# Performance work log

Hardware: AMD Instinct MI355X
Metric: run time of the kernel (lower is better)

The kernel has to match this reference:

```python
import jax, jax.numpy as jnp
import numpy as np

B = 8192
INPUT_DIM = 1024
HIDDEN = 4096
LATENT = 256
K = 16384  # codebook size
COMMIT = 0.25


def setup_inputs() -> dict:
    key = jax.random.key(0)
    ks = jax.random.split(key, 12)

    def lin(k, fan_in, fan_out):
        bound = 1.0 / np.sqrt(fan_in)
        kw, kb = jax.random.split(k)
        W = jax.random.uniform(kw, (fan_in, fan_out), jnp.float32, -bound, bound)
        b = jax.random.uniform(kb, (fan_out,), jnp.float32, -bound, bound)
        return W, b

    eW1, eb1 = lin(ks[0], INPUT_DIM, HIDDEN)
    eW2, eb2 = lin(ks[1], HIDDEN, HIDDEN)
    eW3, eb3 = lin(ks[2], HIDDEN, LATENT)
    dW1, db1 = lin(ks[3], LATENT, HIDDEN)
    dW2, db2 = lin(ks[4], HIDDEN, HIDDEN)
    dW3, db3 = lin(ks[5], HIDDEN, INPUT_DIM)
    codebook = jax.random.uniform(ks[6], (K, LATENT), jnp.float32, -1.0 / K, 1.0 / K)
    x = jax.random.normal(ks[7], (B, INPUT_DIM), jnp.float32)
    return {
        "x": x,
        "eW1": eW1, "eb1": eb1, "eW2": eW2, "eb2": eb2, "eW3": eW3, "eb3": eb3,
        "codebook": codebook,
        "dW1": dW1, "db1": db1, "dW2": dW2, "db2": db2, "dW3": dW3, "db3": db3,
    }


def _encoder(x, eW1, eb1, eW2, eb2, eW3, eb3):
    h = jax.nn.relu(x @ eW1 + eb1)          # dropout is identity in eval
    h = jax.nn.relu(h @ eW2 + eb2)
    return jnp.tanh(h @ eW3 + eb3)          # [B, LATENT]


def _decoder(z, dW1, db1, dW2, db2, dW3, db3):
    h = jax.nn.relu(z @ dW1 + db1)
    h = jax.nn.relu(h @ dW2 + db2)
    return h @ dW3 + db3                    # [B, INPUT_DIM]


def _vq(z, codebook):
    # pairwise squared distances: ||z||^2 + ||e||^2 - 2 z.e^T   -> [B, K]
    d = (jnp.sum(z * z, axis=1, keepdims=True)
         + jnp.sum(codebook * codebook, axis=1)
         - 2.0 * (z @ codebook.T))
    idx = jnp.argmin(d, axis=1)                              # [B]
    enc = jax.nn.one_hot(idx, K, dtype=jnp.float32)          # [B, K]
    q = enc @ codebook                                       # [B, LATENT]
    e_loss = jnp.mean((jax.lax.stop_gradient(q) - z) ** 2)
    q_loss = jnp.mean((q - jax.lax.stop_gradient(z)) ** 2)
    vq_loss = q_loss + COMMIT * e_loss
    q_st = z + jax.lax.stop_gradient(q - z)                  # straight-through
    avg_probs = jnp.mean(enc, axis=0)
    perplexity = jnp.exp(-jnp.sum(avg_probs * jnp.log(avg_probs + 1e-10)))
    return q_st, idx, vq_loss, perplexity


def reference(x, eW1, eb1, eW2, eb2, eW3, eb3, codebook,
              dW1, db1, dW2, db2, dW3, db3):
    z = _encoder(x, eW1, eb1, eW2, eb2, eW3, eb3)
    q, tokens, vq_loss, perplexity = _vq(z, codebook)
    recon = _decoder(q, dW1, db1, dW2, db2, dW3, db3)
    recon_loss = jnp.mean((recon - x) ** 2)
    total = vq_loss + recon_loss
    return recon, tokens, vq_loss, recon_loss, total, perplexity
```

## Files before the change

### kernel.cpp

```cpp
#include <hip/hip_runtime.h>
#include <stdint.h>

#define B_N 8192
#define D_IN 1024
#define D_HID 4096
#define D_LAT 256
#define K_CB 16384

typedef __attribute__((ext_vector_type(8))) short bf16x8;
typedef __attribute__((ext_vector_type(4))) float f32x4;

__device__ __forceinline__ unsigned short f2b(float v) {
  unsigned u = __float_as_uint(v);
  u += 0x7fffu + ((u >> 16) & 1u);
  return (unsigned short)(u >> 16);
}

__global__ __launch_bounds__(256, 2) void enc_big_k(
    const float* __restrict__ A, const float* __restrict__ Bm,
    const float* __restrict__ bias, float* __restrict__ C, int M, int N,
    int K) {
  __shared__ float As[16 * 260];
  __shared__ float Bs[16 * 128];
  const int tid = threadIdx.x;
  const int w = tid >> 6;
  const int tx = tid & 15, ty = tid >> 4;
  int bx = blockIdx.x, by = blockIdx.y;
  {
    const int gx = gridDim.x, n = gx * gridDim.y;
    const int wg = by * gx + bx;
    const int q = n >> 3;
    const int s = (wg & 7) * q + (wg >> 3);
    bx = s % gx;
    by = s / gx;
  }
  const int m0 = by << 8, n0 = bx << 7;

  float acc[16][8];
#pragma unroll
  for (int i = 0; i < 16; ++i)
#pragma unroll
    for (int j = 0; j < 8; ++j) acc[i][j] = 0.0f;

  for (int k0 = 0; k0 < K; k0 += 16) {
#pragma unroll
    for (int r = 0; r < 4; ++r) {
      const int f = tid + (r << 8);
      const int m = f >> 2, kq = (f & 3) << 2;
      const float4 v = *(const float4*)(A + (size_t)(m0 + m) * K + k0 + kq);
      As[(kq + 0) * 260 + m] = v.x;
      As[(kq + 1) * 260 + m] = v.y;
      As[(kq + 2) * 260 + m] = v.z;
      As[(kq + 3) * 260 + m] = v.w;
    }
#pragma unroll
    for (int r = 0; r < 2; ++r) {
      const int f = tid + (r << 8);
      const float* gp = Bm + (size_t)(k0 + (f >> 5)) * N + n0 + ((f & 31) << 2);
      __builtin_amdgcn_global_load_lds((const unsigned int*)gp,
                                       (unsigned int*)&Bs[(r << 10) + (w << 8)],
                                       16, 0, 0);
    }
    __syncthreads();
#pragma unroll
    for (int kk = 0; kk < 16; ++kk) {
      float a[16], b[8];
#pragma unroll
      for (int q = 0; q < 4; ++q)
        *(float4*)(a + (q << 2)) =
            *(const float4*)(&As[kk * 260 + (q << 6) + (ty << 2)]);
      *(float4*)(b) = *(const float4*)(&Bs[kk * 128 + (tx << 2)]);
      *(float4*)(b + 4) = *(const float4*)(&Bs[kk * 128 + 64 + (tx << 2)]);
#pragma unroll
      for (int i = 0; i < 16; ++i)
#pragma unroll
        for (int j = 0; j < 8; ++j) acc[i][j] = fmaf(a[i], b[j], acc[i][j]);
    }
    __syncthreads();
  }

  float bb[8];
  *(float4*)(bb) = *(const float4*)(bias + n0 + (tx << 2));
  *(float4*)(bb + 4) = *(const float4*)(bias + n0 + 64 + (tx << 2));
#pragma unroll
  for (int i = 0; i < 16; ++i) {
    const int row = m0 + ((i >> 2) << 6) + (ty << 2) + (i & 3);
    float vrow[8];
#pragma unroll
    for (int j = 0; j < 8; ++j) vrow[j] = fmaxf(acc[i][j] + bb[j], 0.0f);
    *(float4*)(C + (size_t)row * N + n0 + (tx << 2)) = *(float4*)(vrow);
    *(float4*)(C + (size_t)row * N + n0 + 64 + (tx << 2)) = *(float4*)(vrow + 4);
  }
}

__global__ __launch_bounds__(256, 2) void enc_small_k(
    const float* __restrict__ A, const float* __restrict__ Bm,
    const float* __restrict__ bias, float* __restrict__ C, int M, int N,
    int K) {
  __shared__ float As[16][128];
  __shared__ float Bs[16][128];
  const int tid = threadIdx.x;
  const int tx = tid & 15, ty = tid >> 4;
  const int m0 = blockIdx.y << 7, n0 = blockIdx.x << 7;
  float acc[8][8];
#pragma unroll
  for (int i = 0; i < 8; ++i)
#pragma unroll
    for (int j = 0; j < 8; ++j) acc[i][j] = 0.0f;
  for (int k0 = 0; k0 < K; k0 += 16) {
#pragma unroll
    for (int r = 0; r < 2; ++r) {
      const int f = tid + (r << 8);
      const int m = f >> 2, kq = (f & 3) << 2;
      const float4 v = *(const float4*)(A + (size_t)(m0 + m) * K + k0 + kq);
      As[kq + 0][m] = v.x; As[kq + 1][m] = v.y;
      As[kq + 2][m] = v.z; As[kq + 3][m] = v.w;
    }
#pragma unroll
    for (int r = 0; r < 2; ++r) {
      const int f = tid + (r << 8);
      const int k = f >> 5, nq = (f & 31) << 2;
      *(float4*)(&Bs[k][nq]) =
          *(const float4*)(Bm + (size_t)(k0 + k) * N + n0 + nq);
    }
    __syncthreads();
#pragma unroll
    for (int kk = 0; kk < 16; ++kk) {
      float a[8], b[8];
      *(float4*)(a) = *(const float4*)(&As[kk][ty << 2]);
      *(float4*)(a + 4) = *(const float4*)(&As[kk][64 + (ty << 2)]);
      *(float4*)(b) = *(const float4*)(&Bs[kk][tx << 2]);
      *(float4*)(b + 4) = *(const float4*)(&Bs[kk][64 + (tx << 2)]);
#pragma unroll
      for (int i = 0; i < 8; ++i)
#pragma unroll
        for (int j = 0; j < 8; ++j) acc[i][j] = fmaf(a[i], b[j], acc[i][j]);
    }
    __syncthreads();
  }
  float bb[8];
  *(float4*)(bb) = *(const float4*)(bias + n0 + (tx << 2));
  *(float4*)(bb + 4) = *(const float4*)(bias + n0 + 64 + (tx << 2));
#pragma unroll
  for (int i = 0; i < 8; ++i) {
    const int row = m0 + ((i < 4) ? (ty << 2) + i : 64 + (ty << 2) + i - 4);
    float vrow[8];
#pragma unroll
    for (int j = 0; j < 8; ++j) vrow[j] = fmaxf(acc[i][j] + bb[j], 0.0f);
    *(float4*)(C + (size_t)row * N + n0 + (tx << 2)) = *(float4*)(vrow);
    *(float4*)(C + (size_t)row * N + n0 + 64 + (tx << 2)) = *(float4*)(vrow + 4);
  }
}

__global__ __launch_bounds__(256, 2) void enc3_part_k(
    const float* __restrict__ A, const float* __restrict__ B,
    float* __restrict__ P, int M, int K) {
  __shared__ float As[16][128];
  __shared__ float Bs[16][128];
  const int tid = threadIdx.x;
  const int tx = tid & 15, ty = tid >> 4;
  const int m0 = blockIdx.y << 7, n0 = blockIdx.x << 7;
  const int s = blockIdx.z;
  const int kbeg = s * (K >> 2), kend = kbeg + (K >> 2);
  float acc[8][8];
#pragma unroll
  for (int i = 0; i < 8; ++i)
#pragma unroll
    for (int j = 0; j < 8; ++j) acc[i][j] = 0.0f;
  for (int k0 = kbeg; k0 < kend; k0 += 16) {
#pragma unroll
    for (int r = 0; r < 2; ++r) {
      const int f = tid + (r << 8);
      const int m = f >> 2, kq = (f & 3) << 2;
      const float4 v = *(const float4*)(A + (size_t)(m0 + m) * K + k0 + kq);
      As[kq + 0][m] = v.x; As[kq + 1][m] = v.y;
      As[kq + 2][m] = v.z; As[kq + 3][m] = v.w;
    }
#pragma unroll
    for (int r = 0; r < 2; ++r) {
      const int f = tid + (r << 8);
      const int k = f >> 5, nq = (f & 31) << 2;
      *(float4*)(&Bs[k][nq]) =
          *(const float4*)(B + (size_t)(k0 + k) * D_LAT + n0 + nq);
    }
    __syncthreads();
#pragma unroll
    for (int kk = 0; kk < 16; ++kk) {
      float a[8], b[8];
      *(float4*)(a) = *(const float4*)(&As[kk][ty << 2]);
      *(float4*)(a + 4) = *(const float4*)(&As[kk][64 + (ty << 2)]);
      *(float4*)(b) = *(const float4*)(&Bs[kk][tx << 2]);
      *(float4*)(b + 4) = *(const float4*)(&Bs[kk][64 + (tx << 2)]);
#pragma unroll
      for (int i = 0; i < 8; ++i)
#pragma unroll
        for (int j = 0; j < 8; ++j) acc[i][j] = fmaf(a[i], b[j], acc[i][j]);
    }
    __syncthreads();
  }
  float* Ps = P + (size_t)s * M * D_LAT;
#pragma unroll
  for (int i = 0; i < 8; ++i) {
    const int row = m0 + ((i < 4) ? (ty << 2) + i : 64 + (ty << 2) + i - 4);
    *(float4*)(Ps + (size_t)row * D_LAT + n0 + (tx << 2)) = *(float4*)(&acc[i][0]);
    *(float4*)(Ps + (size_t)row * D_LAT + n0 + 64 + (tx << 2)) = *(float4*)(&acc[i][4]);
  }
}

__global__ void enc3_comb_k(const float* __restrict__ P,
                            const float* __restrict__ bias,
                            float* __restrict__ z, int M) {
  const size_t i4 = (size_t)blockIdx.x * blockDim.x + threadIdx.x;
  const size_t tot = (size_t)M * (D_LAT / 4);
  if (i4 >= tot) return;
  const size_t sstr = (size_t)M * (D_LAT / 4);
  const float4* Pv = (const float4*)P;
  float4 v = Pv[i4];
  const float4 v1 = Pv[i4 + sstr];
  const float4 v2 = Pv[i4 + 2 * sstr];
  const float4 v3 = Pv[i4 + 3 * sstr];
  const int col = (int)((i4 << 2) & (D_LAT - 1));
  const float4 bb = *(const float4*)(bias + col);
  float4 o;
  o.x = tanhf(((v.x + v1.x) + v2.x) + v3.x + bb.x);
  o.y = tanhf(((v.y + v1.y) + v2.y) + v3.y + bb.y);
  o.z = tanhf(((v.z + v1.z) + v2.z) + v3.z + bb.z);
  o.w = tanhf(((v.w + v1.w) + v2.w) + v3.w + bb.w);
  ((float4*)z)[i4] = o;
}

__global__ __launch_bounds__(256, 2) void vq_k(
    const float* __restrict__ A, const float* __restrict__ Bm,
    const float* __restrict__ zz, const float* __restrict__ ee,
    unsigned long long* __restrict__ keys) {
  __shared__ float As[16][128];
  __shared__ float Bs[16][128];
  const int tid = threadIdx.x;
  const int tx = tid & 15, ty = tid >> 4;
  const int m0 = blockIdx.y << 7, n0 = blockIdx.x << 7;
  const int K = D_LAT;
  float acc[8][8];
#pragma unroll
  for (int i = 0; i < 8; ++i)
#pragma unroll
    for (int j = 0; j < 8; ++j) acc[i][j] = 0.0f;
  for (int k0 = 0; k0 < K; k0 += 16) {
#pragma unroll
    for (int r = 0; r < 2; ++r) {
      const int f = tid + (r << 8);
      const int m = f >> 2, kq = (f & 3) << 2;
      const float4 v = *(const float4*)(A + (size_t)(m0 + m) * K + k0 + kq);
      As[kq + 0][m] = v.x; As[kq + 1][m] = v.y;
      As[kq + 2][m] = v.z; As[kq + 3][m] = v.w;
    }
#pragma unroll
    for (int r = 0; r < 2; ++r) {
      const int f = tid + (r << 8);
      const int n = f >> 2, kq = (f & 3) << 2;
      const float4 v = *(const float4*)(Bm + (size_t)(n0 + n) * K + k0 + kq);
      Bs[kq + 0][n] = v.x; Bs[kq + 1][n] = v.y;
      Bs[kq + 2][n] = v.z; Bs[kq + 3][n] = v.w;
    }
    __syncthreads();
#pragma unroll
    for (int kk = 0; kk < 16; ++kk) {
      float a[8], b[8];
      *(float4*)(a) = *(const float4*)(&As[kk][ty << 2]);
      *(float4*)(a + 4) = *(const float4*)(&As[kk][64 + (ty << 2)]);
      *(float4*)(b) = *(const float4*)(&Bs[kk][tx << 2]);
      *(float4*)(b + 4) = *(const float4*)(&Bs[kk][64 + (tx << 2)]);
#pragma unroll
      for (int i = 0; i < 8; ++i)
#pragma unroll
        for (int j = 0; j < 8; ++j) acc[i][j] = fmaf(a[i], b[j], acc[i][j]);
    }
    __syncthreads();
  }
  float zr[8];
#pragma unroll
  for (int i = 0; i < 8; ++i)
    zr[i] = zz[m0 + ((i < 4) ? (ty << 2) + i : 64 + (ty << 2) + i - 4)];
  float ev[8];
  *(float4*)(ev) = *(const float4*)(ee + n0 + (tx << 2));
  *(float4*)(ev + 4) = *(const float4*)(ee + n0 + 64 + (tx << 2));
#pragma unroll
  for (int i = 0; i < 8; ++i) {
    unsigned long long bk = ~0ull;
#pragma unroll
    for (int j = 0; j < 8; ++j) {
      const int col = n0 + ((j < 4) ? (tx << 2) + j : 64 + (tx << 2) + j - 4);
      const float t = zr[i] + ev[j];
      const float d = t - 2.0f * acc[i][j];
      unsigned u = __float_as_uint(d);
      u = (u & 0x80000000u) ? ~u : (u | 0x80000000u);
      const unsigned long long key = ((unsigned long long)u << 32) | (unsigned)col;
      bk = key < bk ? key : bk;
    }
#pragma unroll
    for (int s = 1; s <= 8; s <<= 1) {
      const unsigned long long o = __shfl_xor(bk, s);
      if (o < bk) bk = o;
    }
    if (tx == 0) {
      const int row = m0 + ((i < 4) ? (ty << 2) + i : 64 + (ty << 2) + i - 4);
      atomicMin(keys + row, bk);
    }
  }
}

template <int EPI>
__device__ __forceinline__ void mgemm_body(
    const unsigned short* __restrict__ A, const unsigned short* __restrict__ Bt,
    const float* __restrict__ bias, void* __restrict__ Cout, int M, int N,
    int K, const float* __restrict__ xref, double* __restrict__ accums) {
  __shared__ __align__(16) unsigned short As[4096];
  __shared__ __align__(16) unsigned short Bs[4096];
  const int tid = threadIdx.x;
  const int w = tid >> 6, l = tid & 63;
  const int wr = w >> 1, wc = w & 1;
  const int g = l >> 4, tx = l & 15;
  const int m0 = blockIdx.y << 7, n0 = blockIdx.x << 7;

  f32x4 acc[4][4];
#pragma unroll
  for (int i = 0; i < 4; ++i)
#pragma unroll
    for (int j = 0; j < 4; ++j) acc[i][j] = (f32x4)0.0f;

  for (int k0 = 0; k0 < K; k0 += 32) {
#pragma unroll
    for (int c = 0; c < 2; ++c) {
      const int f = tid + (c << 8);
      const unsigned short* ga =
          A + (size_t)(m0 + (f >> 2)) * K + k0 + ((f & 3) << 3);
      __builtin_amdgcn_global_load_lds((const unsigned int*)ga,
                                       (unsigned int*)&As[(c << 11) + (w << 9)],
                                       16, 0, 0);
      const unsigned short* gb =
          Bt + (size_t)(n0 + (f >> 2)) * K + k0 + ((f & 3) << 3);
      __builtin_amdgcn_global_load_lds((const unsigned int*)gb,
                                       (unsigned int*)&Bs[(c << 11) + (w << 9)],
                                       16, 0, 0);
    }
    __syncthreads();
    bf16x8 af[4], bfv[4];
#pragma unroll
    for (int f = 0; f < 4; ++f) {
      af[f] = *(const bf16x8*)&As[((wr << 6) + (f << 4) + tx) * 32 + (g << 3)];
      bfv[f] = *(const bf16x8*)&Bs[((wc << 6) + (f << 4) + tx) * 32 + (g << 3)];
    }
#pragma unroll
    for (int fm = 0; fm < 4; ++fm)
#pragma unroll
      for (int fn = 0; fn < 4; ++fn)
        acc[fm][fn] = __builtin_amdgcn_mfma_f32_16x16x32_bf16(
            af[fm], bfv[fn], acc[fm][fn], 0, 0, 0);
    __syncthreads();
  }

  double lsum = 0.0;
#pragma unroll
  for (int fm = 0; fm < 4; ++fm) {
    const int row0 = m0 + (wr << 6) + (fm << 4) + (g << 2);
#pragma unroll
    for (int fn = 0; fn < 4; ++fn) {
      const int col = n0 + (wc << 6) + (fn << 4) + tx;
      const float bb = bias[col];
#pragma unroll
      for (int r = 0; r < 4; ++r) {
        float v = acc[fm][fn][r] + bb;
        if (EPI == 0) {
          v = fmaxf(v, 0.0f);
          ((unsigned short*)Cout)[(size_t)(row0 + r) * N + col] = f2b(v);
        } else {
          const float xr = xref[(size_t)(row0 + r) * N + col];
          const float df = v - xr;
          lsum += (double)df * (double)df;
          ((float*)Cout)[(size_t)(row0 + r) * N + col] = v;
        }
      }
    }
  }
  if (EPI == 1) {
#pragma unroll
    for (int o = 32; o; o >>= 1) lsum += __shfl_down(lsum, o);
    if (l == 0) atomicAdd(accums + 1, lsum);
  }
}

__global__ __launch_bounds__(256, 2) void dec_relu_k(
    const unsigned short* A, const unsigned short* Bt, const float* bias,
    unsigned short* Cout, int M, int N, int K) {
  mgemm_body<0>(A, Bt, bias, Cout, M, N, K, nullptr, nullptr);
}
__global__ __launch_bounds__(256, 2) void dec_recon_k(
    const unsigned short* A, const unsigned short* Bt, const float* bias,
    float* Cout, int M, int N, int K, const float* xref, double* accums) {
  mgemm_body<1>(A, Bt, bias, Cout, M, N, K, xref, accums);
}

__global__ void castT_k(const float* __restrict__ W,
                        unsigned short* __restrict__ out, int K, int N) {
  __shared__ float t[32][33];
  const int tx = threadIdx.x & 31, ty4 = threadIdx.x >> 5;
  const int nb = blockIdx.x << 5, kb = blockIdx.y << 5;
#pragma unroll
  for (int r = 0; r < 4; ++r) {
    const int k = (ty4 << 2) + r;
    t[k][tx] = W[(size_t)(kb + k) * N + nb + tx];
  }
  __syncthreads();
#pragma unroll
  for (int r = 0; r < 4; ++r) {
    const int n = (ty4 << 2) + r;
    out[(size_t)(nb + n) * K + kb + tx] = f2b(t[tx][n]);
  }
}

__global__ void rowsumsq(const float* __restrict__ v, float* __restrict__ out,
                         int rows) {
  const int w = (int)((blockIdx.x * blockDim.x + threadIdx.x) >> 6);
  const int lane = threadIdx.x & 63;
  if (w >= rows) return;
  const float4 x = *(const float4*)(v + (size_t)w * 256 + (lane << 2));
  float s = ((x.x * x.x + x.y * x.y) + x.z * x.z) + x.w * x.w;
#pragma unroll
  for (int o = 32; o; o >>= 1) s += __shfl_down(s, o);
  if (lane == 0) out[w] = s;
}

__global__ void finalize_vq(const unsigned long long* __restrict__ keys,
                            const float* __restrict__ z,
                            const float* __restrict__ cb,
                            unsigned short* __restrict__ qst_bf,
                            float* __restrict__ tok, int* __restrict__ counts,
                            double* __restrict__ accums) {
  const int row = (int)((blockIdx.x * blockDim.x + threadIdx.x) >> 6);
  const int lane = threadIdx.x & 63;
  if (row >= B_N) return;
  const int idx = (int)(keys[row] & 0xffffffffull);
  const float4 zv = *(const float4*)(z + (size_t)row * 256 + (lane << 2));
  const float4 evv = *(const float4*)(cb + (size_t)idx * 256 + (lane << 2));
  float4 q;
  double s = 0.0;
  float d;
  d = evv.x - zv.x; q.x = zv.x + d; s += (double)d * (double)d;
  d = evv.y - zv.y; q.y = zv.y + d; s += (double)d * (double)d;
  d = evv.z - zv.z; q.z = zv.z + d; s += (double)d * (double)d;
  d = evv.w - zv.w; q.w = zv.w + d; s += (double)d * (double)d;
  ushort4 qb;
  qb.x = f2b(q.x); qb.y = f2b(q.y); qb.z = f2b(q.z); qb.w = f2b(q.w);
  *(ushort4*)(qst_bf + (size_t)row * 256 + (lane << 2)) = qb;
#pragma unroll
  for (int o = 32; o; o >>= 1) s += __shfl_down(s, o);
  if (lane == 0) {
    atomicAdd(accums + 0, s);
    tok[row] = (float)idx;
    atomicAdd(counts + idx, 1);
  }
}

__global__ void finalize_scalars(const int* __restrict__ counts,
                                 const double* __restrict__ accums,
                                 float* __restrict__ outs) {
  __shared__ double red[256];
  double h = 0.0;
  for (int k = threadIdx.x; k < K_CB; k += 256) {
    const float p = (float)counts[k] * (1.0f / 8192.0f);
    const float t = p * logf(p + 1e-10f);
    h += (double)t;
  }
  red[threadIdx.x] = h;
  __syncthreads();
  for (int s = 128; s; s >>= 1) {
    if ((int)threadIdx.x < s) red[threadIdx.x] += red[threadIdx.x + s];
    __syncthreads();
  }
  if (threadIdx.x == 0) {
    const float perp = expf((float)(-red[0]));
    const float m1 = (float)(accums[0] * (1.0 / ((double)B_N * (double)D_LAT)));
    const float vq = m1 + 0.25f * m1;
    const float rl = (float)(accums[1] * (1.0 / ((double)B_N * (double)D_IN)));
    outs[0] = vq;
    outs[1] = rl;
    outs[2] = vq + rl;
    outs[3] = perp;
  }
}

extern "C" void kernel_launch(void* const* d_in, const int* in_sizes, int n_in,
                              void* d_out, int out_size, void* d_ws,
                              size_t ws_size, hipStream_t stream) {
  (void)in_sizes; (void)n_in; (void)out_size;
  const float* x   = (const float*)d_in[0];
  const float* eW1 = (const float*)d_in[1];
  const float* eb1 = (const float*)d_in[2];
  const float* eW2 = (const float*)d_in[3];
  const float* eb2 = (const float*)d_in[4];
  const float* eW3 = (const float*)d_in[5];
  const float* eb3 = (const float*)d_in[6];
  const float* cb  = (const float*)d_in[7];
  const float* dW1 = (const float*)d_in[8];
  const float* db1 = (const float*)d_in[9];
  const float* dW2 = (const float*)d_in[10];
  const float* db2 = (const float*)d_in[11];
  const float* dW3 = (const float*)d_in[12];
  const float* db3 = (const float*)d_in[13];
  float* out = (float*)d_out;

  char* ws = (char*)d_ws;
  const size_t OFF_Z      = 0;
  const size_t OFF_EEV    = OFF_Z + (size_t)B_N * D_LAT * 4;
  const size_t OFF_ZZV    = OFF_EEV + (size_t)K_CB * 4;
  const size_t OFF_KEYS   = OFF_ZZV + (size_t)B_N * 4;
  const size_t OFF_COUNTS = OFF_KEYS + (size_t)B_N * 8;
  const size_t OFF_ACC    = OFF_COUNTS + (size_t)K_CB * 4;
  const size_t OFF_QB     = OFF_ACC + 256;
  const size_t OFF_H      = OFF_QB + (size_t)B_N * D_LAT * 2;

  float* z    = (float*)(ws + OFF_Z);
  float* eev  = (float*)(ws + OFF_EEV);
  float* zzv  = (float*)(ws + OFF_ZZV);
  unsigned long long* keys = (unsigned long long*)(ws + OFF_KEYS);
  int* counts = (int*)(ws + OFF_COUNTS);
  double* accums = (double*)(ws + OFF_ACC);
  unsigned short* qst_bf = (unsigned short*)(ws + OFF_QB);

  int c_enc = 256;
  for (int c = 8192; c >= 256; c >>= 1)
    if (OFF_H + 2ull * c * D_HID * 4 <= ws_size) { c_enc = c; break; }
  float* hA = (float*)(ws + OFF_H);
  float* hB = hA + (size_t)c_enc * D_HID;
  float* P3 = hA;

  const size_t SZ_WB1 = (size_t)D_HID * D_LAT * 2;
  const size_t SZ_WB2 = (size_t)D_HID * D_HID * 2;
  const size_t SZ_WB3 = (size_t)D_IN * D_HID * 2;
  const size_t OFF_DECH = OFF_H + SZ_WB1 + SZ_WB2 + SZ_WB3;
  int c_dec = 128;
  for (int c = 8192; c >= 128; c >>= 1)
    if (OFF_DECH + 2ull * c * D_HID * 2 <= ws_size) { c_dec = c; break; }
  unsigned short* wB1 = (unsigned short*)(ws + OFF_H);
  unsigned short* wB2 = (unsigned short*)(ws + OFF_H + SZ_WB1);
  unsigned short* wB3 = (unsigned short*)(ws + OFF_H + SZ_WB1 + SZ_WB2);
  unsigned short* hbfA = (unsigned short*)(ws + OFF_DECH);
  unsigned short* hbfB = hbfA + (size_t)c_dec * D_HID;

  float* tok_out = out + (size_t)B_N * D_IN;
  float* scal_out = tok_out + B_N;

  hipMemsetAsync(keys, 0xFF, (size_t)B_N * 8, stream);
  hipMemsetAsync(counts, 0, (size_t)K_CB * 4, stream);
  hipMemsetAsync(accums, 0, 2 * sizeof(double), stream);

  rowsumsq<<<(K_CB * 64) / 256, 256, 0, stream>>>(cb, eev, K_CB);

  const bool big = (c_enc >= 4096);
  for (int c0 = 0; c0 < B_N; c0 += c_enc) {
    if (big) {
      const dim3 gH(D_HID / 128, c_enc / 256);
      enc_big_k<<<gH, 256, 0, stream>>>(x + (size_t)c0 * D_IN, eW1, eb1, hA,
                                        c_enc, D_HID, D_IN);
      enc_big_k<<<gH, 256, 0, stream>>>(hA, eW2, eb2, hB, c_enc, D_HID, D_HID);
    } else {
      const dim3 gH(D_HID / 128, c_enc / 128);
      enc_small_k<<<gH, 256, 0, stream>>>(x + (size_t)c0 * D_IN, eW1, eb1, hA,
                                          c_enc, D_HID, D_IN);
      enc_small_k<<<gH, 256, 0, stream>>>(hA, eW2, eb2, hB, c_enc, D_HID,
                                          D_HID);
    }
    enc3_part_k<<<dim3(D_LAT / 128, c_enc / 128, 4), 256, 0, stream>>>(
        hB, eW3, P3, c_enc, D_HID);
    enc3_comb_k<<<(c_enc * (D_LAT / 4) + 255) / 256, 256, 0, stream>>>(
        P3, eb3, z + (size_t)c0 * D_LAT, c_enc);
  }

  rowsumsq<<<(B_N * 64) / 256, 256, 0, stream>>>(z, zzv, B_N);

  vq_k<<<dim3(K_CB / 128, B_N / 128), 256, 0, stream>>>(z, cb, zzv, eev, keys);
  finalize_vq<<<(B_N * 64) / 256, 256, 0, stream>>>(keys, z, cb, qst_bf,
                                                    tok_out, counts, accums);

  castT_k<<<dim3(D_HID / 32, D_LAT / 32), 256, 0, stream>>>(dW1, wB1, D_LAT, D_HID);
  castT_k<<<dim3(D_HID / 32, D_HID / 32), 256, 0, stream>>>(dW2, wB2, D_HID, D_HID);
  castT_k<<<dim3(D_IN / 32, D_HID / 32), 256, 0, stream>>>(dW3, wB3, D_HID, D_IN);

  for (int c0 = 0; c0 < B_N; c0 += c_dec) {
    const dim3 gH(D_HID / 128, c_dec / 128);
    dec_relu_k<<<gH, 256, 0, stream>>>(qst_bf + (size_t)c0 * D_LAT, wB1, db1,
                                       hbfA, c_dec, D_HID, D_LAT);
    dec_relu_k<<<gH, 256, 0, stream>>>(hbfA, wB2, db2, hbfB, c_dec, D_HID,
                                       D_HID);
    dec_recon_k<<<dim3(D_IN / 128, c_dec / 128), 256, 0, stream>>>(
        hbfB, wB3, db3, out + (size_t)c0 * D_IN, c_dec, D_IN, D_HID,
        x + (size_t)c0 * D_IN, accums);
  }

  finalize_scalars<<<1, 256, 0, stream>>>(counts, accums, scal_out);
}
```

Measured before the change: 5.612 ms.

## Enlarge VQ distance tile, split encoder layer-3 K eight ways, swizzle decoder blocks

The VQ distance kernel now uses 256x128 tiles with 16x8 per-thread accumulators and padded shared memory. The larger tile improves register reuse and halves the number of codebook reloads. The encoder's third layer splits K into 8 partial sums instead of 4 to raise parallelism, and the combine kernel now sums 8 partials. The XCD block swizzle is factored into a macro and also applied to the bf16 decoder GEMMs and the VQ kernel for better L2 locality. In exchange there is higher register pressure, more partial-sum traffic and a changed fp32 summation order.

```diff
diff --git a/kernel.cpp b/kernel.cpp
--- a/kernel.cpp
+++ b/kernel.cpp
@@ -15,6 +15,16 @@
   u += 0x7fffu + ((u >> 16) & 1u);
   return (unsigned short)(u >> 16);
 }
+
+#define XCD_SWIZZLE(bx, by)                                   \
+  {                                                           \
+    const int gx_ = gridDim.x, n_ = gx_ * gridDim.y;          \
+    const int wg_ = (by)*gx_ + (bx);                          \
+    const int q_ = n_ >> 3;                                   \
+    const int s_ = (wg_ & 7) * q_ + (wg_ >> 3);               \
+    (bx) = s_ % gx_;                                          \
+    (by) = s_ / gx_;                                          \
+  }
 
 __global__ __launch_bounds__(256, 2) void enc_big_k(
     const float* __restrict__ A, const float* __restrict__ Bm,
@@ -26,14 +36,7 @@
   const int w = tid >> 6;
   const int tx = tid & 15, ty = tid >> 4;
   int bx = blockIdx.x, by = blockIdx.y;
-  {
-    const int gx = gridDim.x, n = gx * gridDim.y;
-    const int wg = by * gx + bx;
-    const int q = n >> 3;
-    const int s = (wg & 7) * q + (wg >> 3);
-    bx = s % gx;
-    by = s / gx;
-  }
+  XCD_SWIZZLE(bx, by)
   const int m0 = by << 8, n0 = bx << 7;
 
   float acc[16][8];
@@ -161,7 +164,7 @@
   const int tx = tid & 15, ty = tid >> 4;
   const int m0 = blockIdx.y << 7, n0 = blockIdx.x << 7;
   const int s = blockIdx.z;
-  const int kbeg = s * (K >> 2), kend = kbeg + (K >> 2);
+  const int kbeg = s * (K >> 3), kend = kbeg + (K >> 3);
   float acc[8][8];
 #pragma unroll
   for (int i = 0; i < 8; ++i)
@@ -215,80 +218,93 @@
   if (i4 >= tot) return;
   const size_t sstr = (size_t)M * (D_LAT / 4);
   const float4* Pv = (const float4*)P;
-  float4 v = Pv[i4];
-  const float4 v1 = Pv[i4 + sstr];
-  const float4 v2 = Pv[i4 + 2 * sstr];
-  const float4 v3 = Pv[i4 + 3 * sstr];
+  float sx = 0.f, sy = 0.f, sz = 0.f, sw = 0.f;
+#pragma unroll
+  for (int s = 0; s < 8; ++s) {
+    const float4 v = Pv[i4 + (size_t)s * sstr];
+    sx += v.x; sy += v.y; sz += v.z; sw += v.w;
+  }
   const int col = (int)((i4 << 2) & (D_LAT - 1));
   const float4 bb = *(const float4*)(bias + col);
   float4 o;
-  o.x = tanhf(((v.x + v1.x) + v2.x) + v3.x + bb.x);
-  o.y = tanhf(((v.y + v1.y) + v2.y) + v3.y + bb.y);
-  o.z = tanhf(((v.z + v1.z) + v2.z) + v3.z + bb.z);
-  o.w = tanhf(((v.w + v1.w) + v2.w) + v3.w + bb.w);
+  o.x = tanhf(sx + bb.x);
+  o.y = tanhf(sy + bb.y);
+  o.z = tanhf(sz + bb.z);
+  o.w = tanhf(sw + bb.w);
   ((float4*)z)[i4] = o;
 }
 
-__global__ __launch_bounds__(256, 2) void vq_k(
+__global__ __launch_bounds__(256, 2) void vq_k256(
     const float* __restrict__ A, const float* __restrict__ Bm,
     const float* __restrict__ zz, const float* __restrict__ ee,
     unsigned long long* __restrict__ keys) {
-  __shared__ float As[16][128];
-  __shared__ float Bs[16][128];
+  __shared__ float As[16 * 260];
+  __shared__ float Bs[16 * 132];
   const int tid = threadIdx.x;
   const int tx = tid & 15, ty = tid >> 4;
-  const int m0 = blockIdx.y << 7, n0 = blockIdx.x << 7;
+  int bx = blockIdx.x, by = blockIdx.y;
+  XCD_SWIZZLE(bx, by)
+  const int m0 = by << 8, n0 = bx << 7;
   const int K = D_LAT;
-  float acc[8][8];
-#pragma unroll
-  for (int i = 0; i < 8; ++i)
+
+  float acc[16][8];
+#pragma unroll
+  for (int i = 0; i < 16; ++i)
 #pragma unroll
     for (int j = 0; j < 8; ++j) acc[i][j] = 0.0f;
+
   for (int k0 = 0; k0 < K; k0 += 16) {
 #pragma unroll
-    for (int r = 0; r < 2; ++r) {
+    for (int r = 0; r < 4; ++r) {
       const int f = tid + (r << 8);
       const int m = f >> 2, kq = (f & 3) << 2;
       const float4 v = *(const float4*)(A + (size_t)(m0 + m) * K + k0 + kq);
-      As[kq + 0][m] = v.x; As[kq + 1][m] = v.y;
-      As[kq + 2][m] = v.z; As[kq + 3][m] = v.w;
+      As[(kq + 0) * 260 + m] = v.x;
+      As[(kq + 1) * 260 + m] = v.y;
+      As[(kq + 2) * 260 + m] = v.z;
+      As[(kq + 3) * 260 + m] = v.w;
     }
 #pragma unroll
     for (int r = 0; r < 2; ++r) {
       const int f = tid + (r << 8);
       const int n = f >> 2, kq = (f & 3) << 2;
       const float4 v = *(const float4*)(Bm + (size_t)(n0 + n) * K + k0 + kq);
-      Bs[kq + 0][n] = v.x; Bs[kq + 1][n] = v.y;
-      Bs[kq + 2][n] = v.z; Bs[kq + 3][n] = v.w;
+      Bs[(kq + 0) * 132 + n] = v.x;
+      Bs[(kq + 1) * 132 + n] = v.y;
+      Bs[(kq + 2) * 132 + n] = v.z;
+      Bs[(kq + 3) * 132 + n] = v.w;
     }
     __syncthreads();
 #pragma unroll
     for (int kk = 0; kk < 16; ++kk) {
-      float a[8], b[8];
-      *(float4*)(a) = *(const float4*)(&As[kk][ty << 2]);
-      *(float4*)(a + 4) = *(const float4*)(&As[kk][64 + (ty << 2)]);
-      *(float4*)(b) = *(const float4*)(&Bs[kk][tx << 2]);
-      *(float4*)(b + 4) = *(const float4*)(&Bs[kk][64 + (tx << 2)]);
-#pragma unroll
-      for (int i = 0; i < 8; ++i)
+      float a[16], b[8];
+#pragma unroll
+      for (int q = 0; q < 4; ++q)
+        *(float4*)(a + (q << 2)) =
+            *(const float4*)(&As[kk * 260 + (q << 6) + (ty << 2)]);
+      *(float4*)(b) = *(const float4*)(&Bs[kk * 132 + (tx << 2)]);
+      *(float4*)(b + 4) = *(const float4*)(&Bs[kk * 132 + 64 + (tx << 2)]);
+#pragma unroll
+      for (int i = 0; i < 16; ++i)
 #pragma unroll
         for (int j = 0; j < 8; ++j) acc[i][j] = fmaf(a[i], b[j], acc[i][j]);
     }
     __syncthreads();
   }
-  float zr[8];
-#pragma unroll
-  for (int i = 0; i < 8; ++i)
-    zr[i] = zz[m0 + ((i < 4) ? (ty << 2) + i : 64 + (ty << 2) + i - 4)];
+
+  float zr[16];
+#pragma unroll
+  for (int i = 0; i < 16; ++i)
+    zr[i] = zz[m0 + ((i >> 2) << 6) + (ty << 2) + (i & 3)];
   float ev[8];
   *(float4*)(ev) = *(const float4*)(ee + n0 + (tx << 2));
   *(float4*)(ev + 4) = *(const float4*)(ee + n0 + 64 + (tx << 2));
 #pragma unroll
-  for (int i = 0; i < 8; ++i) {
+  for (int i = 0; i < 16; ++i) {
     unsigned long long bk = ~0ull;
 #pragma unroll
     for (int j = 0; j < 8; ++j) {
-      const int col = n0 + ((j < 4) ? (tx << 2) + j : 64 + (tx << 2) + j - 4);
+      const int col = n0 + ((j >> 2) << 6) + (tx << 2) + (j & 3);
       const float t = zr[i] + ev[j];
       const float d = t - 2.0f * acc[i][j];
       unsigned u = __float_as_uint(d);
@@ -302,7 +318,7 @@
       if (o < bk) bk = o;
     }
     if (tx == 0) {
-      const int row = m0 + ((i < 4) ? (ty << 2) + i : 64 + (ty << 2) + i - 4);
+      const int row = m0 + ((i >> 2) << 6) + (ty << 2) + (i & 3);
       atomicMin(keys + row, bk);
     }
   }
@@ -319,7 +335,9 @@
   const int w = tid >> 6, l = tid & 63;
   const int wr = w >> 1, wc = w & 1;
   const int g = l >> 4, tx = l & 15;
-  const int m0 = blockIdx.y << 7, n0 = blockIdx.x << 7;
+  int bx = blockIdx.x, by = blockIdx.y;
+  XCD_SWIZZLE(bx, by)
+  const int m0 = by << 7, n0 = bx << 7;
 
   f32x4 acc[4][4];
 #pragma unroll
@@ -569,7 +587,7 @@
       enc_small_k<<<gH, 256, 0, stream>>>(hA, eW2, eb2, hB, c_enc, D_HID,
                                           D_HID);
     }
-    enc3_part_k<<<dim3(D_LAT / 128, c_enc / 128, 4), 256, 0, stream>>>(
+    enc3_part_k<<<dim3(D_LAT / 128, c_enc / 128, 8), 256, 0, stream>>>(
         hB, eW3, P3, c_enc, D_HID);
     enc3_comb_k<<<(c_enc * (D_LAT / 4) + 255) / 256, 256, 0, stream>>>(
         P3, eb3, z + (size_t)c0 * D_LAT, c_enc);
@@ -577,7 +595,8 @@
 
   rowsumsq<<<(B_N * 64) / 256, 256, 0, stream>>>(z, zzv, B_N);
 
-  vq_k<<<dim3(K_CB / 128, B_N / 128), 256, 0, stream>>>(z, cb, zzv, eev, keys);
+  vq_k256<<<dim3(K_CB / 128, B_N / 256), 256, 0, stream>>>(z, cb, zzv, eev,
+                                                           keys);
   finalize_vq<<<(B_N * 64) / 256, 256, 0, stream>>>(keys, z, cb, qst_bf,
                                                     tok_out, counts, accums);
 
```

Result: no change. 5.562 ms (-0.9%).
